# Performance work log

Hardware: AMD Instinct MI355X
Metric: run time of the kernel (lower is better)

Reference implementation:

```python
import jax, jax.numpy as jnp
import numpy as np

M1, M2, BS = 2000, 400, 8
AT = M1 + M2
E1, E2, E3 = 60000, 20000, 20000
H, F, NG, L, C = 64, 64, 50, 4, 4
CUTOFF = 10.0
LOG2 = 0.6931471805599453  # shift of ShiftedSoftplus


def _ssp(x):
    return jax.nn.softplus(x) - LOG2


def _smear(d):
    # GaussianSmearing(0, cutoff, NG)
    offset = jnp.linspace(0.0, CUTOFF, NG)
    coeff = -0.5 / (offset[1] - offset[0]) ** 2
    return jnp.exp(coeff * (d[:, None] - offset[None, :]) ** 2)  # [E, NG]


def _colored_mlp(attr, colors, w1, b1, w2, b2):
    # w1:[C,NG,F] b1:[C,F] w2:[C,F,F] b2:[C,F]; route each edge through its color's MLP
    out = jnp.zeros((attr.shape[0], w1.shape[-1]), attr.dtype)
    for c in range(C):  # fixed small color count
        h = _ssp(attr @ w1[c] + b1[c]) @ w2[c] + b2[c]
        out = out + jnp.where((colors == c)[:, None], h, jnp.zeros((), attr.dtype))
    return out


def _block(h, ei, ew, attr, col, p):
    # InteractionBlock: CFConv -> ssp -> linear
    mw1, mb1, mw2, mb2, cw1, cw2, cb2, bw, bb = p
    Ccut = 0.5 * (jnp.cos(ew * jnp.pi / CUTOFF) + 1.0)
    W = _colored_mlp(attr, col, mw1, mb1, mw2, mb2) * Ccut[:, None]  # [E,F]
    x = h @ cw1                                   # lin1 (no bias) [N,F]
    msg = x[ei[:, 0]] * W                         # gather x_j, modulate
    agg = jax.ops.segment_sum(msg, ei[:, 1], num_segments=h.shape[0])  # scatter-add
    x = agg @ cw2 + cb2                           # lin2
    return _ssp(x) @ bw + bb                      # act + block linear


def _batch_graph(ei, ew, col):
    # replicate per-structure edges across the batch with node offset b*AT
    offs = (jnp.arange(BS, dtype=ei.dtype) * AT)[:, None, None]
    ei_b = (ei[None] + offs).reshape(-1, 2)
    return ei_b, jnp.tile(ew, BS), jnp.tile(col, BS)


def _forward(sites, sites_p, e1, ew1, c1, e2, ew2, c2, e3, ew3, c3,
             emb_w, emb_p_w, mlp_w1, mlp_b1, mlp_w2, mlp_b2,
             conv_w1, conv_w2, conv_b2, blk_w, blk_b,
             out_w1, out_b1, out_w2, out_b2):
    h = jnp.concatenate([emb_w[sites], emb_p_w[sites_p]], axis=1).reshape(BS * AT, H)
    graphs = []
    for (ei, ew, col) in ((e1, ew1, c1), (e2, ew2, c2), (e3, ew3, c3)):
        ei_b, ew_b, col_b = _batch_graph(ei, ew, col)
        graphs.append((ei_b, ew_b, col_b, _smear(ew_b)))
    for l in range(L):
        delta = jnp.zeros_like(h)
        for g, (ei_b, ew_b, col_b, attr_b) in enumerate(graphs):
            p = (mlp_w1[l, g], mlp_b1[l, g], mlp_w2[l, g], mlp_b2[l, g],
                 conv_w1[l, g], conv_w2[l, g], conv_b2[l, g], blk_w[l, g], blk_b[l, g])
            delta = delta + _block(h, ei_b, ew_b, attr_b, col_b, p)
        h = h + delta
    hp = h.reshape(BS, AT, H)[:, M1:, :]   # mask selects pore nodes only
    o = hp @ out_w1 + out_b1               # NB: original has `h - self.act(h)` no-op, so no activation here
    o = o @ out_w2 + out_b2                # [BS, M2, 1]
    return o.sum(axis=1)                   # 'add' readout per batch -> [BS, 1]


def setup_inputs() -> dict:
    key = jax.random.key(0)
    ks = jax.random.split(key, 24)
    f = lambda i, shape, s=0.1: jax.random.normal(ks[i], shape, jnp.float32) * s
    sites = jax.random.randint(ks[0], (BS, M1), 0, 1, dtype=jnp.int32)
    sites_p = jax.random.randint(ks[1], (BS, M2), 0, 2, dtype=jnp.int32)
    e1 = jax.random.randint(ks[2], (E1, 2), 0, M1, dtype=jnp.int32)
    e2 = jnp.stack([jax.random.randint(ks[3], (E2,), 0, M1, dtype=jnp.int32),
                    jax.random.randint(ks[4], (E2,), M1, AT, dtype=jnp.int32)], 1)
    e3 = jnp.stack([jax.random.randint(ks[5], (E3,), M1, AT, dtype=jnp.int32),
                    jax.random.randint(ks[6], (E3,), 0, M1, dtype=jnp.int32)], 1)
    ew1 = jax.random.uniform(ks[7], (E1,), jnp.float32, 0.5, CUTOFF)
    ew2 = jax.random.uniform(ks[8], (E2,), jnp.float32, 0.5, CUTOFF)
    ew3 = jax.random.uniform(ks[9], (E3,), jnp.float32, 0.5, CUTOFF)
    c1 = jax.random.randint(ks[10], (E1,), 0, C, dtype=jnp.int32)
    c2 = jax.random.randint(ks[11], (E2,), 0, C, dtype=jnp.int32)
    c3 = jax.random.randint(ks[12], (E3,), 0, C, dtype=jnp.int32)
    return {
        'sites': sites, 'sites_p': sites_p,
        'edge_idx1': e1, 'edge_weight1': ew1, 'colors1': c1,
        'edge_idx2': e2, 'edge_weight2': ew2, 'colors2': c2,
        'edge_idx3': e3, 'edge_weight3': ew3, 'colors3': c3,
        'emb_w': f(13, (1, H), 1.0), 'emb_p_w': f(14, (2, H), 1.0),
        'mlp_w1': f(15, (L, 3, C, NG, F)), 'mlp_b1': jnp.zeros((L, 3, C, F), jnp.float32),
        'mlp_w2': f(16, (L, 3, C, F, F)), 'mlp_b2': jnp.zeros((L, 3, C, F), jnp.float32),
        'conv_w1': f(17, (L, 3, H, F)), 'conv_w2': f(18, (L, 3, F, H)),
        'conv_b2': jnp.zeros((L, 3, H), jnp.float32),
        'blk_w': f(19, (L, 3, H, H)), 'blk_b': jnp.zeros((L, 3, H), jnp.float32),
        'out_w1': f(20, (H, H // 2)), 'out_b1': jnp.zeros((H // 2,), jnp.float32),
        'out_w2': f(21, (H // 2, 1)), 'out_b2': jnp.zeros((1,), jnp.float32),
    }


def reference(sites, sites_p, edge_idx1, edge_weight1, colors1,
              edge_idx2, edge_weight2, colors2, edge_idx3, edge_weight3, colors3,
              emb_w, emb_p_w, mlp_w1, mlp_b1, mlp_w2, mlp_b2,
              conv_w1, conv_w2, conv_b2, blk_w, blk_b,
              out_w1, out_b1, out_w2, out_b2):
    return _forward(sites, sites_p, edge_idx1, edge_weight1, colors1,
                    edge_idx2, edge_weight2, colors2, edge_idx3, edge_weight3, colors3,
                    emb_w, emb_p_w, mlp_w1, mlp_b1, mlp_w2, mlp_b2,
                    conv_w1, conv_w2, conv_b2, blk_w, blk_b,
                    out_w1, out_b1, out_w2, out_b2)
```

## Files before the change

### kernel.cpp

```cpp
#include <hip/hip_runtime.h>
#include <math.h>

constexpr int M1 = 2000, M2 = 400, BS = 8;
constexpr int AT = M1 + M2;
constexpr int NN = BS * AT;
constexpr int E1 = 60000, E2 = 20000, E3 = 20000;
constexpr int ET = E1 + E2 + E3;
constexpr int H = 64, F = 64, NG = 50, L = 4, C = 4;
constexpr float CUTOFF = 10.0f;
constexpr float LOG2F_ = 0.6931471805599453f;

constexpr float SMEAR_STEP = 10.0f / 49.0f;
constexpr float SMEAR_COEFF = -12.005f;
constexpr float PI_OVER_CUT = 0.31415926535897932f;

constexpr int NBLK = (ET + 255) / 256;

constexpr int NT = 256;
constexpr float DSCALE = (float)(NT - 1) / CUTOFF;

constexpr int GP0 = E1 + 3 * M1;
constexpr int GP1 = E2 + 3 * M2;
constexpr int GP2 = E3 + 3 * M1;
constexpr int ETP = GP0 + GP1 + GP2;

constexpr int TILE_M = 32;

constexpr int GU  = 4400;
constexpr int GBLK = GU / 4;
constexpr int SITE_T = M1 / 4;
constexpr int PORE_T = M2 / 4;
constexpr int NTILE  = SITE_T + PORE_T;

constexpr int LT0 = M1 / 4;
constexpr int LT1 = M1 / 4;
constexpr int LT2 = M2 / 4;
constexpr int LTOT = LT0 + LT1 + LT2;
constexpr int PADB = (3 * AT + 255) / 256;

constexpr int A_TAB  = 192;
constexpr int A_INIT = NN * 64 / 256;
constexpr int A_CNT  = NBLK;
constexpr int A_CV   = 3;
constexpr int A_TOT  = A_TAB + A_INIT + A_CNT + A_CV;
constexpr int B_PACK = 48 * NT * 64 / 256;
constexpr int B_TOT  = B_PACK + 3;

constexpr size_t O_HA    = 0;
constexpr size_t O_HB    = O_HA  + (size_t)NN * 64 * 4;
constexpr size_t O_XG    = O_HB  + (size_t)NN * 64 * 4;
constexpr size_t O_MSG   = O_XG  + (size_t)3 * AT * 512 * 2;
constexpr size_t O_TABF  = O_MSG + (size_t)3 * 8 * AT * 64 * 4;
constexpr size_t O_TAB2  = O_TABF + (size_t)48 * NT * 64 * 4;
constexpr size_t O_EDATA = O_TAB2 + (size_t)48 * NT * 64 * 4;
constexpr size_t O_INT   = O_EDATA + (size_t)ETP * 16;
constexpr int I_DEG  = 0;
constexpr int I_CUR  = 7200;
constexpr int I_ZEND = 14400;
constexpr int I_BASE = 14400;
constexpr int I_CV   = 21616;

__device__ inline float sspf(float x) {
    return fmaxf(x, 0.0f) + log1pf(expf(-fabsf(x))) - LOG2F_;
}
__device__ inline float sspf_fast(float x) {
    float t = __expf(-fabsf(x));
    return fmaxf(x, 0.0f) + __logf(1.0f + t) - LOG2F_;
}

__device__ inline unsigned int bf16rn(float x) {
    unsigned int u = __float_as_uint(x);
    u = (u + 0x7FFFu + ((u >> 16) & 1u)) >> 16;
    return u & 0xFFFFu;
}

__device__ inline int graph_off(int g) { return g == 0 ? 0 : (g == 1 ? GP0 : GP0 + GP1); }

__device__ inline void edge_decode(int idx, int& g, int& e,
                                   const int* ei1, const int* ei2, const int* ei3,
                                   const int* c1, const int* c2, const int* c3,
                                   const int*& ei, const int*& cl) {
    if (idx < E1)            { g = 0; e = idx;           ei = ei1; cl = c1; }
    else if (idx < E1 + E2)  { g = 1; e = idx - E1;      ei = ei2; cl = c2; }
    else                     { g = 2; e = idx - E1 - E2; ei = ei3; cl = c3; }
}

__global__ __launch_bounds__(256) void k_setupA(
    const float* __restrict__ mlp_w1, const float* __restrict__ mlp_b1,
    const float* __restrict__ mlp_w2, const float* __restrict__ mlp_b2,
    float* __restrict__ tabF,
    const int* __restrict__ sites, const int* __restrict__ sites_p,
    const float* __restrict__ emb_w, const float* __restrict__ emb_p_w,
    float* __restrict__ h,
    const int* __restrict__ ei1, const int* __restrict__ ei2,
    const int* __restrict__ ei3, const int* __restrict__ c1,
    const int* __restrict__ c2, const int* __restrict__ c3,
    int* __restrict__ deg,
    const float* __restrict__ conv_b2, const float* __restrict__ blk_w,
    const float* __restrict__ blk_b, float* __restrict__ cvbuf) {
    int bid = blockIdx.x;
    int t = threadIdx.x;
    if (bid < A_TAB) {
        const int lane = t & 63;
        int wslot = bid * 4 + (t >> 6);
        int s = wslot >> 4;
        int pq = wslot & 15;
        int l = s % L;
        int gc = s / L;
        int c = gc % C;
        int g = gc / C;
        size_t wb = (size_t)((l * 3 + g) * C + c);
        const float* w1 = mlp_w1 + wb * NG * F;
        const float* w2 = mlp_w2 + wb * F * F;
        float w1c[NG], w2c[F];
        #pragma unroll
        for (int k = 0; k < NG; k++) w1c[k] = w1[k * F + lane];
        #pragma unroll
        for (int k = 0; k < F; k++) w2c[k] = w2[k * F + lane];
        float b1c = mlp_b1[wb * F + lane];
        float b2c = mlp_b2[wb * F + lane];
        for (int pp = 0; pp < 16; pp++) {
            int p = pq * 16 + pp;
            float d = (float)p * (CUTOFF / (float)(NT - 1));
            float dd = d - (float)lane * SMEAR_STEP;
            float av = (lane < NG) ? __expf(SMEAR_COEFF * dd * dd) : 0.0f;
            float acc = b1c;
            #pragma unroll
            for (int k = 0; k < NG; k++) acc = fmaf(__shfl(av, k), w1c[k], acc);
            float tt = sspf_fast(acc);
            float acc2 = b2c;
            #pragma unroll
            for (int j = 0; j < F; j++) acc2 = fmaf(__shfl(tt, j), w2c[j], acc2);
            float ccut = 0.5f * (__cosf(d * PI_OVER_CUT) + 1.0f);
            tabF[((size_t)s * NT + p) * 64 + lane] = acc2 * ccut;
        }
    } else if (bid < A_TAB + A_INIT) {
        int idx = (bid - A_TAB) * 256 + t;
        int f = idx & 63;
        int n = idx >> 6;
        int b = n / AT;
        int i = n - b * AT;
        float v;
        if (i < M1) v = emb_w[sites[b * M1 + i] * H + f];
        else        v = emb_p_w[sites_p[b * M2 + (i - M1)] * H + f];
        h[idx] = v;
    } else if (bid < A_TAB + A_INIT + A_CNT) {
        int idx = (bid - A_TAB - A_INIT) * 256 + t;
        if (idx < ET) {
            int g, e; const int* ei; const int* cl;
            edge_decode(idx, g, e, ei1, ei2, ei3, c1, c2, c3, ei, cl);
            atomicAdd(&deg[g * AT + ei[2 * e + 1]], 1);
        }
    } else {
        int s = (bid - A_TAB - A_INIT - A_CNT) * 4 + (t >> 6);
        int lane = t & 63;
        if (s < 12) {
            float sl = sspf(conv_b2[s * 64 + lane]);
            const float* bw = blk_w + (size_t)s * 4096;
            float a = blk_b[s * 64 + lane];
            #pragma unroll 8
            for (int k = 0; k < 64; k++)
                a = fmaf(__shfl(sl, k), bw[k * 64 + lane], a);
            cvbuf[s * 64 + lane] = a;
        }
    }
}

__global__ __launch_bounds__(256) void k_setupB(
    const float* __restrict__ tabF, unsigned int* __restrict__ tab2,
    const int* __restrict__ deg, int* __restrict__ base) {
    int bid = blockIdx.x;
    int t = threadIdx.x;
    if (bid < B_PACK) {
        int idx = bid * 256 + t;
        int pc = idx & (NT * 64 - 1);
        int nxt = (pc < (NT - 1) * 64) ? idx + 64 : idx;
        unsigned int lo = bf16rn(tabF[idx]);
        unsigned int hi = bf16rn(tabF[nxt]);
        tab2[idx] = lo | (hi << 16);
    } else {
        const int T = 256, CH = 10;
        __shared__ int lsum[256];
        int g = bid - B_PACK;
        int loc[CH];
        int s = 0;
        #pragma unroll
        for (int i = 0; i < CH; i++) {
            int idx = t * CH + i;
            int v = (idx < AT) ? ((deg[g * AT + idx] + 3) & ~3) : 0;
            loc[i] = s;
            s += v;
        }
        lsum[t] = s;
        __syncthreads();
        for (int off = 1; off < T; off <<= 1) {
            int v = 0;
            if (t >= off) v = lsum[t - off];
            __syncthreads();
            lsum[t] += v;
            __syncthreads();
        }
        int tb = lsum[t] - s;
        #pragma unroll
        for (int i = 0; i < CH; i++) {
            int idx = t * CH + i;
            if (idx < AT) base[g * (AT + 1) + idx] = tb + loc[i];
        }
        if (t == T - 1) base[g * (AT + 1) + AT] = lsum[T - 1];
    }
}

__device__ inline void fma4(float acc[4], float a, const float4 b) {
    acc[0] = fmaf(a, b.x, acc[0]);
    acc[1] = fmaf(a, b.y, acc[1]);
    acc[2] = fmaf(a, b.z, acc[2]);
    acc[3] = fmaf(a, b.w, acc[3]);
}

__device__ inline void stage_B(const float* __restrict__ gB, float (*Bs)[68], int t) {
    #pragma unroll
    for (int i = 0; i < 4; i++) {
        int v = t + i * 256;
        int r = v >> 4, c4 = (v & 15) * 4;
        *(float4*)&Bs[r][c4] = *(const float4*)(gB + (size_t)r * 64 + c4);
    }
}
struct WReg { float4 v0, v1, v2, v3; };
__device__ inline WReg stage_ld(const float* __restrict__ g, int t) {
    int r0 = t >> 4, c4 = (t & 15) * 4;
    WReg w;
    w.v0 = *(const float4*)(g + (size_t)r0 * 64 + c4);
    w.v1 = *(const float4*)(g + (size_t)(r0 + 16) * 64 + c4);
    w.v2 = *(const float4*)(g + (size_t)(r0 + 32) * 64 + c4);
    w.v3 = *(const float4*)(g + (size_t)(r0 + 48) * 64 + c4);
    return w;
}
__device__ inline void stage_st(const WReg& w, float (*Bs)[68], int t) {
    int r0 = t >> 4, c4 = (t & 15) * 4;
    *(float4*)&Bs[r0][c4]      = w.v0;
    *(float4*)&Bs[r0 + 16][c4] = w.v1;
    *(float4*)&Bs[r0 + 32][c4] = w.v2;
    *(float4*)&Bs[r0 + 48][c4] = w.v3;
}

__device__ inline void gemm_tile(const float (*As)[68], const float (*Bs)[68],
                                 int r0, int c0, float acc0[4], float acc1[4]) {
    #pragma unroll 4
    for (int k0 = 0; k0 < 64; k0 += 4) {
        float4 a0 = *(const float4*)&As[r0][k0];
        float4 a1 = *(const float4*)&As[r0 + 1][k0];
        float4 b0 = *(const float4*)&Bs[k0][c0];
        float4 b1 = *(const float4*)&Bs[k0 + 1][c0];
        float4 b2 = *(const float4*)&Bs[k0 + 2][c0];
        float4 b3 = *(const float4*)&Bs[k0 + 3][c0];
        fma4(acc0, a0.x, b0); fma4(acc0, a0.y, b1);
        fma4(acc0, a0.z, b2); fma4(acc0, a0.w, b3);
        fma4(acc1, a1.x, b0); fma4(acc1, a1.y, b1);
        fma4(acc1, a1.z, b2); fma4(acc1, a1.w, b3);
    }
}

__device__ inline void xg_transpose_store(const float (*T)[68],
                                          unsigned short* __restrict__ xg,
                                          int g, int i0, int t) {
    int k = t >> 6, c = t & 63;
    unsigned int w0 = bf16rn(T[k * 8 + 0][c]) | (bf16rn(T[k * 8 + 1][c]) << 16);
    unsigned int w1 = bf16rn(T[k * 8 + 2][c]) | (bf16rn(T[k * 8 + 3][c]) << 16);
    unsigned int w2 = bf16rn(T[k * 8 + 4][c]) | (bf16rn(T[k * 8 + 5][c]) << 16);
    unsigned int w3 = bf16rn(T[k * 8 + 6][c]) | (bf16rn(T[k * 8 + 7][c]) << 16);
    unsigned short* out = xg + (((size_t)g * AT + i0 + k) * 64 + c) * 8;
    *(uint4*)out = make_uint4(w0, w1, w2, w3);
}

__device__ inline float tab_lerp(unsigned int u, int z) {
    float lo = __uint_as_float(u << 16);
    float hi = __uint_as_float(u & 0xFFFF0000u);
    return fmaf(__int_as_float(z), hi - lo, lo);
}
__device__ inline void gmadd8(float acc[8], uint4 q, float wl) {
    acc[0] = fmaf(__uint_as_float(q.x << 16),         wl, acc[0]);
    acc[1] = fmaf(__uint_as_float(q.x & 0xFFFF0000u), wl, acc[1]);
    acc[2] = fmaf(__uint_as_float(q.y << 16),         wl, acc[2]);
    acc[3] = fmaf(__uint_as_float(q.y & 0xFFFF0000u), wl, acc[3]);
    acc[4] = fmaf(__uint_as_float(q.z << 16),         wl, acc[4]);
    acc[5] = fmaf(__uint_as_float(q.z & 0xFFFF0000u), wl, acc[5]);
    acc[6] = fmaf(__uint_as_float(q.w << 16),         wl, acc[6]);
    acc[7] = fmaf(__uint_as_float(q.w & 0xFFFF0000u), wl, acc[7]);
}

__global__ __launch_bounds__(256) void k_gather(
    const int4* __restrict__ edata, const int* __restrict__ base,
    const unsigned int* __restrict__ tab2,
    const unsigned short* __restrict__ xg,
    float* __restrict__ msg, int l) {
    const int t = threadIdx.x;
    const int lane = t & 63;
    const int u = blockIdx.x * 4 + (t >> 6);
    int g, dst;
    if (u < M1)           { g = 0; dst = u; }
    else if (u < AT)      { g = 1; dst = u; }
    else                  { g = 2; dst = u - AT; }
    const int s = base[g * (AT + 1) + dst];
    const int e = base[g * (AT + 1) + dst + 1];
    const int4* ed = edata + graph_off(g);
    const unsigned int* tg = tab2 + ((size_t)g * C * L + l) * NT * 64;
    const unsigned short* xgg = xg + (size_t)g * AT * 512;
    float acc[8];
    #pragma unroll
    for (int j = 0; j < 8; j++) acc[j] = 0.0f;
    for (int i = s; i < e; i += 4) {
        int4 e0 = ed[i];
        int4 e1 = ed[i + 1];
        int4 e2 = ed[i + 2];
        int4 e3 = ed[i + 3];
        unsigned int u0 = tg[(size_t)e0.y * 64 + lane];
        unsigned int u1 = tg[(size_t)e1.y * 64 + lane];
        unsigned int u2 = tg[(size_t)e2.y * 64 + lane];
        unsigned int u3 = tg[(size_t)e3.y * 64 + lane];
        uint4 q0 = *(const uint4*)(xgg + ((size_t)e0.x * 64 + lane) * 8);
        uint4 q1 = *(const uint4*)(xgg + ((size_t)e1.x * 64 + lane) * 8);
        uint4 q2 = *(const uint4*)(xgg + ((size_t)e2.x * 64 + lane) * 8);
        uint4 q3 = *(const uint4*)(xgg + ((size_t)e3.x * 64 + lane) * 8);
        gmadd8(acc, q0, tab_lerp(u0, e0.z));
        gmadd8(acc, q1, tab_lerp(u1, e1.z));
        gmadd8(acc, q2, tab_lerp(u2, e2.z));
        gmadd8(acc, q3, tab_lerp(u3, e3.z));
    }
    float* mp = msg + ((size_t)g * 8 * AT + dst) * 64 + lane;
    #pragma unroll
    for (int b = 0; b < 8; b++) mp[(size_t)b * AT * 64] = acc[b];
}

__global__ __launch_bounds__(256) void k_node(
    const float* __restrict__ msg,
    const float* __restrict__ conv_w2, const float* __restrict__ conv_b2,
    const float* __restrict__ blk_w, const float* __restrict__ blk_b,
    const float* __restrict__ conv_w1, const float* __restrict__ cvbuf,
    const float* __restrict__ hIn, float* __restrict__ hOut,
    unsigned short* __restrict__ xg, int l, int last) {
    __shared__ float As[TILE_M][68];
    __shared__ float Ps[TILE_M][68];
    __shared__ float Bs[64][68];
    const int t = threadIdx.x;
    const int bid = blockIdx.x;
    const int site = (bid < SITE_T) ? 1 : 0;
    const int i0 = site ? bid * 4 : M1 + (bid - SITE_T) * 4;
    const int gA = site ? 0 : 1;
    const size_t pbA = (size_t)(l * 3 + gA);
    const size_t pbB = (size_t)(l * 3 + 2);

    WReg R = stage_ld(conv_w2 + pbA * 4096, t);
    #pragma unroll
    for (int it = 0; it < 2; it++) {
        int v = t + it * 256;
        int r = v >> 4, c4 = (v & 15) * 4;
        int k = r >> 3, b = r & 7;
        *(float4*)&As[r][c4] =
            *(const float4*)(msg + (((size_t)gA * 8 + b) * AT + i0 + k) * 64 + c4);
    }
    stage_st(R, Bs, t);
    R = stage_ld(blk_w + pbA * 4096, t);
    __syncthreads();

    const int cg = t & 15, rg = t >> 4;
    const int c0 = cg * 4, r0 = rg * 2;
    const float* cvl = cvbuf + (size_t)l * 3 * 64;

    float4 cb = *(const float4*)(conv_b2 + pbA * 64 + c0);
    float x0[4] = {cb.x, cb.y, cb.z, cb.w};
    float x1[4] = {cb.x, cb.y, cb.z, cb.w};
    gemm_tile(As, Bs, r0, c0, x0, x1);
    __syncthreads();
    *(float4*)&As[r0][c0] =
        make_float4(sspf(x0[0]), sspf(x0[1]), sspf(x0[2]), sspf(x0[3]));
    *(float4*)&As[r0 + 1][c0] =
        make_float4(sspf(x1[0]), sspf(x1[1]), sspf(x1[2]), sspf(x1[3]));
    stage_st(R, Bs, t);
    if (site) R = stage_ld(conv_w2 + pbB * 4096, t);
    else if (!last) R = stage_ld(conv_w1 + (size_t)((l + 1) * 3 + 2) * 4096, t);
    __syncthreads();

    const int k0r = r0 >> 3, b0r = r0 & 7;
    const size_t o0 = ((size_t)b0r * AT + i0 + k0r) * 64 + c0;
    const int k1r = (r0 + 1) >> 3, b1r = (r0 + 1) & 7;
    const size_t o1 = ((size_t)b1r * AT + i0 + k1r) * 64 + c0;
    float4 h0 = *(const float4*)(hIn + o0);
    float4 h1 = *(const float4*)(hIn + o1);
    float4 bbA = *(const float4*)(blk_b + pbA * 64 + c0);
    float4 ex;
    if (site) {
        float4 bbB = *(const float4*)(blk_b + pbB * 64 + c0);
        float4 cv1 = *(const float4*)(cvl + 64 + c0);
        ex = make_float4(bbB.x + cv1.x, bbB.y + cv1.y, bbB.z + cv1.z, bbB.w + cv1.w);
    } else {
        float4 cv0 = *(const float4*)(cvl + c0);
        float4 cv2 = *(const float4*)(cvl + 128 + c0);
        ex = make_float4(cv0.x + cv2.x, cv0.y + cv2.y, cv0.z + cv2.z, cv0.w + cv2.w);
    }
    float d0[4] = {h0.x + bbA.x + ex.x, h0.y + bbA.y + ex.y,
                   h0.z + bbA.z + ex.z, h0.w + bbA.w + ex.w};
    float d1[4] = {h1.x + bbA.x + ex.x, h1.y + bbA.y + ex.y,
                   h1.z + bbA.z + ex.z, h1.w + bbA.w + ex.w};
    gemm_tile(As, Bs, r0, c0, d0, d1);

    if (site) {
        __syncthreads();
        #pragma unroll
        for (int it = 0; it < 2; it++) {
            int v = t + it * 256;
            int r = v >> 4, c4 = (v & 15) * 4;
            int k = r >> 3, b = r & 7;
            *(float4*)&As[r][c4] =
                *(const float4*)(msg + (((size_t)2 * 8 + b) * AT + i0 + k) * 64 + c4);
        }
        stage_st(R, Bs, t);
        R = stage_ld(blk_w + pbB * 4096, t);
        __syncthreads();
        float4 cb2v = *(const float4*)(conv_b2 + pbB * 64 + c0);
        float y0[4] = {cb2v.x, cb2v.y, cb2v.z, cb2v.w};
        float y1[4] = {cb2v.x, cb2v.y, cb2v.z, cb2v.w};
        gemm_tile(As, Bs, r0, c0, y0, y1);
        __syncthreads();
        *(float4*)&As[r0][c0] =
            make_float4(sspf(y0[0]), sspf(y0[1]), sspf(y0[2]), sspf(y0[3]));
        *(float4*)&As[r0 + 1][c0] =
            make_float4(sspf(y1[0]), sspf(y1[1]), sspf(y1[2]), sspf(y1[3]));
        stage_st(R, Bs, t);
        if (!last) R = stage_ld(conv_w1 + (size_t)((l + 1) * 3 + 0) * 4096, t);
        __syncthreads();
        gemm_tile(As, Bs, r0, c0, d0, d1);
    }
    *(float4*)(hOut + o0) = make_float4(d0[0], d0[1], d0[2], d0[3]);
    *(float4*)(hOut + o1) = make_float4(d1[0], d1[1], d1[2], d1[3]);
    if (last) return;

    __syncthreads();
    *(float4*)&As[r0][c0]     = make_float4(d0[0], d0[1], d0[2], d0[3]);
    *(float4*)&As[r0 + 1][c0] = make_float4(d1[0], d1[1], d1[2], d1[3]);
    stage_st(R, Bs, t);
    if (site) R = stage_ld(conv_w1 + (size_t)((l + 1) * 3 + 1) * 4096, t);
    __syncthreads();
    float p0[4] = {0, 0, 0, 0}, p1[4] = {0, 0, 0, 0};
    gemm_tile(As, Bs, r0, c0, p0, p1);
    __syncthreads();
    *(float4*)&Ps[r0][c0]     = make_float4(p0[0], p0[1], p0[2], p0[3]);
    *(float4*)&Ps[r0 + 1][c0] = make_float4(p1[0], p1[1], p1[2], p1[3]);
    if (site) stage_st(R, Bs, t);
    __syncthreads();
    xg_transpose_store(Ps, xg, site ? 0 : 2, i0, t);
    if (site) {
        float q0[4] = {0, 0, 0, 0}, q1[4] = {0, 0, 0, 0};
        gemm_tile(As, Bs, r0, c0, q0, q1);
        __syncthreads();
        *(float4*)&Ps[r0][c0]     = make_float4(q0[0], q0[1], q0[2], q0[3]);
        *(float4*)&Ps[r0 + 1][c0] = make_float4(q1[0], q1[1], q1[2], q1[3]);
        __syncthreads();
        xg_transpose_store(Ps, xg, 1, i0, t);
    }
}

__global__ __launch_bounds__(256) void k_fl(
    const int* __restrict__ ei1, const int* __restrict__ ei2,
    const int* __restrict__ ei3, const int* __restrict__ c1,
    const int* __restrict__ c2, const int* __restrict__ c3,
    const float* __restrict__ ew1, const float* __restrict__ ew2,
    const float* __restrict__ ew3,
    const int* __restrict__ base, int* __restrict__ cur,
    const int* __restrict__ deg, int4* __restrict__ edata,
    const float* __restrict__ h, const float* __restrict__ conv_w1,
    unsigned short* __restrict__ xg) {
    __shared__ float As[TILE_M][68];
    __shared__ float Bs[64][68];
    int t = threadIdx.x;
    if (blockIdx.x >= LTOT + NBLK) {
        int idx = (blockIdx.x - LTOT - NBLK) * 256 + t;
        if (idx >= 3 * AT) return;
        int g = idx / AT, dn = idx - g * AT;
        int d = deg[g * AT + dn];
        int pd = (d + 3) & ~3;
        int4* ep = edata + graph_off(g) + base[g * (AT + 1) + dn] + d;
        for (int k2 = 0; k2 < pd - d; k2++) ep[k2] = make_int4(0, NT - 1, 0, 0);
        return;
    }
    if (blockIdx.x >= LTOT) {
        int idx = (blockIdx.x - LTOT) * 256 + t;
        if (idx >= ET) return;
        int g, e; const int* ei; const int* cl;
        edge_decode(idx, g, e, ei1, ei2, ei3, c1, c2, c3, ei, cl);
        const float* ew = (g == 0) ? ew1 : (g == 1 ? ew2 : ew3);
        int dst = ei[2 * e + 1];
        int src = ei[2 * e];
        int p = base[g * (AT + 1) + dst] + atomicAdd(&cur[g * AT + dst], 1);
        float tt = ew[e] * DSCALE;
        int i0 = min((int)tt, NT - 2);
        float fr = tt - (float)i0;
        int cb = cl[e] * (L * NT) + i0;
        edata[graph_off(g) + p] = make_int4(src, cb, __float_as_int(fr), 0);
        return;
    }
    int g, igrp;
    {
        int bid = blockIdx.x;
        if (bid < LT0)            { g = 0; igrp = bid; }
        else if (bid < LT0 + LT1) { g = 1; igrp = bid - LT0; }
        else                      { g = 2; igrp = LT0 + (bid - LT0 - LT1); }
    }
    int i0 = igrp * 4;
    #pragma unroll
    for (int it = 0; it < 2; it++) {
        int v = t + it * 256;
        int r = v >> 4, c4 = (v & 15) * 4;
        int n = (r & 7) * AT + i0 + (r >> 3);
        *(float4*)&As[r][c4] = *(const float4*)(h + (size_t)n * 64 + c4);
    }
    stage_B(conv_w1 + (size_t)g * 4096, Bs, t);
    __syncthreads();
    int cg = t & 15, rg = t >> 4;
    int c0 = cg * 4, r0 = rg * 2;
    float acc0[4] = {0, 0, 0, 0}, acc1[4] = {0, 0, 0, 0};
    gemm_tile(As, Bs, r0, c0, acc0, acc1);
    __syncthreads();
    *(float4*)&As[r0][c0]     = make_float4(acc0[0], acc0[1], acc0[2], acc0[3]);
    *(float4*)&As[r0 + 1][c0] = make_float4(acc1[0], acc1[1], acc1[2], acc1[3]);
    __syncthreads();
    xg_transpose_store(As, xg, g, i0, t);
}

__global__ void k_read(const float* __restrict__ h,
                       const float* __restrict__ w1, const float* __restrict__ b1,
                       const float* __restrict__ w2, const float* __restrict__ b2,
                       float* __restrict__ out) {
    int b = blockIdx.x;
    int lane = threadIdx.x & 63;
    int wv = threadIdx.x >> 6;
    __shared__ float part[4];
    float weff = 0.0f;
    #pragma unroll
    for (int j = 0; j < H / 2; j++) weff = fmaf(w1[lane * (H / 2) + j], w2[j], weff);
    float acc = 0.0f;
    for (int i = wv * (M2 / 4); i < (wv + 1) * (M2 / 4); i++)
        acc += h[((size_t)b * AT + M1 + i) * H + lane];
    float v = acc * weff;
    for (int off = 32; off; off >>= 1) v += __shfl_xor(v, off);
    if (lane == 0) part[wv] = v;
    __syncthreads();
    if (threadIdx.x == 0) {
        float bias = b2[0];
        for (int j = 0; j < H / 2; j++) bias = fmaf(b1[j], w2[j], bias);
        out[b] = part[0] + part[1] + part[2] + part[3] + (float)M2 * bias;
    }
}

extern "C" void kernel_launch(void* const* d_in, const int* in_sizes, int n_in,
                              void* d_out, int out_size, void* d_ws, size_t ws_size,
                              hipStream_t stream) {
    const int* sites   = (const int*)d_in[0];
    const int* sites_p = (const int*)d_in[1];
    const int* ei1 = (const int*)d_in[2];
    const float* ew1 = (const float*)d_in[3];
    const int* c1 = (const int*)d_in[4];
    const int* ei2 = (const int*)d_in[5];
    const float* ew2 = (const float*)d_in[6];
    const int* c2 = (const int*)d_in[7];
    const int* ei3 = (const int*)d_in[8];
    const float* ew3 = (const float*)d_in[9];
    const int* c3 = (const int*)d_in[10];
    const float* emb_w   = (const float*)d_in[11];
    const float* emb_p_w = (const float*)d_in[12];
    const float* mlp_w1 = (const float*)d_in[13];
    const float* mlp_b1 = (const float*)d_in[14];
    const float* mlp_w2 = (const float*)d_in[15];
    const float* mlp_b2 = (const float*)d_in[16];
    const float* conv_w1 = (const float*)d_in[17];
    const float* conv_w2 = (const float*)d_in[18];
    const float* conv_b2 = (const float*)d_in[19];
    const float* blk_w = (const float*)d_in[20];
    const float* blk_b = (const float*)d_in[21];
    const float* out_w1 = (const float*)d_in[22];
    const float* out_b1 = (const float*)d_in[23];
    const float* out_w2 = (const float*)d_in[24];
    const float* out_b2 = (const float*)d_in[25];

    char* ws = (char*)d_ws;
    float* hA   = (float*)(ws + O_HA);
    float* hB   = (float*)(ws + O_HB);
    unsigned short* xg = (unsigned short*)(ws + O_XG);
    float* msg  = (float*)(ws + O_MSG);
    float* tabF = (float*)(ws + O_TABF);
    unsigned int* tab2 = (unsigned int*)(ws + O_TAB2);
    int4*  edata = (int4*)(ws + O_EDATA);
    int* ip    = (int*)(ws + O_INT);
    int* deg   = ip + I_DEG;
    int* cur   = ip + I_CUR;
    int* ibase = ip + I_BASE;
    float* cvbuf = (float*)(ip + I_CV);

    hipMemsetAsync(ip, 0, (size_t)I_ZEND * sizeof(int), stream);

    k_setupA<<<A_TOT, 256, 0, stream>>>(mlp_w1, mlp_b1, mlp_w2, mlp_b2, tabF,
                                        sites, sites_p, emb_w, emb_p_w, hA,
                                        ei1, ei2, ei3, c1, c2, c3, deg,
                                        conv_b2, blk_w, blk_b, cvbuf);
    k_setupB<<<B_TOT, 256, 0, stream>>>(tabF, tab2, deg, ibase);
    k_fl<<<LTOT + NBLK + PADB, 256, 0, stream>>>(ei1, ei2, ei3, c1, c2, c3,
                                                 ew1, ew2, ew3, ibase, cur, deg,
                                                 edata, hA, conv_w1, xg);

    float* hcur = hA;
    float* hnxt = hB;
    for (int l = 0; l < L; l++) {
        int last = (l == L - 1) ? 1 : 0;
        k_gather<<<GBLK, 256, 0, stream>>>(edata, ibase, tab2, xg, msg, l);
        k_node<<<NTILE, 256, 0, stream>>>(msg, conv_w2, conv_b2, blk_w, blk_b,
                                          conv_w1, cvbuf, hcur, hnxt, xg, l, last);
        float* tmp = hcur; hcur = hnxt; hnxt = tmp;
    }
    k_read<<<BS, 256, 0, stream>>>(hcur, out_w1, out_b1, out_w2, out_b2, (float*)d_out);
}
```

Measured before the change: 327.1 us.

## Split gather per batch half, fuse table bf16 packing into table kernel

The gather kernel now assigns two wavefronts per destination node, each handling four of the eight batch copies with 8-byte loads, and unrolls the edge loop by eight with a four-edge tail. Edge bounds are made wave-uniform with readfirstlane. The filter-table kernel computes 17 points per wave and writes the packed bf16 pair table directly, removing the fp32 intermediate table and its separate packing pass. The degree scan becomes its own small kernel. The price is that each edge's table entry and edge record are loaded twice, once per half, while the gather gets twice as many waves to hide latency.

```diff
diff --git a/kernel.cpp b/kernel.cpp
--- a/kernel.cpp
+++ b/kernel.cpp
@@ -26,8 +26,7 @@
 
 constexpr int TILE_M = 32;
 
-constexpr int GU  = 4400;
-constexpr int GBLK = GU / 4;
+constexpr int GUB = 8800 / 4;
 constexpr int SITE_T = M1 / 4;
 constexpr int PORE_T = M2 / 4;
 constexpr int NTILE  = SITE_T + PORE_T;
@@ -42,16 +41,13 @@
 constexpr int A_INIT = NN * 64 / 256;
 constexpr int A_CNT  = NBLK;
 constexpr int A_CV   = 3;
-constexpr int A_TOT  = A_TAB + A_INIT + A_CNT + A_CV;
-constexpr int B_PACK = 48 * NT * 64 / 256;
-constexpr int B_TOT  = B_PACK + 3;
+constexpr int A_TOT  = A_INIT + A_CNT + A_CV;
 
 constexpr size_t O_HA    = 0;
 constexpr size_t O_HB    = O_HA  + (size_t)NN * 64 * 4;
 constexpr size_t O_XG    = O_HB  + (size_t)NN * 64 * 4;
 constexpr size_t O_MSG   = O_XG  + (size_t)3 * AT * 512 * 2;
-constexpr size_t O_TABF  = O_MSG + (size_t)3 * 8 * AT * 64 * 4;
-constexpr size_t O_TAB2  = O_TABF + (size_t)48 * NT * 64 * 4;
+constexpr size_t O_TAB2  = O_MSG + (size_t)3 * 8 * AT * 64 * 4;
 constexpr size_t O_EDATA = O_TAB2 + (size_t)48 * NT * 64 * 4;
 constexpr size_t O_INT   = O_EDATA + (size_t)ETP * 16;
 constexpr int I_DEG  = 0;
@@ -85,10 +81,54 @@
     else                     { g = 2; e = idx - E1 - E2; ei = ei3; cl = c3; }
 }
 
-__global__ __launch_bounds__(256) void k_setupA(
+__global__ __launch_bounds__(256) void k_tab(
     const float* __restrict__ mlp_w1, const float* __restrict__ mlp_b1,
     const float* __restrict__ mlp_w2, const float* __restrict__ mlp_b2,
-    float* __restrict__ tabF,
+    unsigned int* __restrict__ tab2) {
+    const int t = threadIdx.x;
+    const int lane = t & 63;
+    int wslot = blockIdx.x * 4 + (t >> 6);
+    int s = wslot >> 4;
+    int pq = wslot & 15;
+    int l = s % L;
+    int gc = s / L;
+    int c = gc % C;
+    int g = gc / C;
+    size_t wb = (size_t)((l * 3 + g) * C + c);
+    const float* w1 = mlp_w1 + wb * NG * F;
+    const float* w2 = mlp_w2 + wb * F * F;
+    float w1c[NG], w2c[F];
+    #pragma unroll
+    for (int k = 0; k < NG; k++) w1c[k] = w1[k * F + lane];
+    #pragma unroll
+    for (int k = 0; k < F; k++) w2c[k] = w2[k * F + lane];
+    float b1c = mlp_b1[wb * F + lane];
+    float b2c = mlp_b2[wb * F + lane];
+    float vals[17];
+    for (int pp = 0; pp <= 16; pp++) {
+        int p = min(pq * 16 + pp, NT - 1);
+        float d = (float)p * (CUTOFF / (float)(NT - 1));
+        float dd = d - (float)lane * SMEAR_STEP;
+        float av = (lane < NG) ? __expf(SMEAR_COEFF * dd * dd) : 0.0f;
+        float acc = b1c;
+        #pragma unroll
+        for (int k = 0; k < NG; k++) acc = fmaf(__shfl(av, k), w1c[k], acc);
+        float tt = sspf_fast(acc);
+        float acc2 = b2c;
+        #pragma unroll
+        for (int j = 0; j < F; j++) acc2 = fmaf(__shfl(tt, j), w2c[j], acc2);
+        float ccut = 0.5f * (__cosf(d * PI_OVER_CUT) + 1.0f);
+        vals[pp] = acc2 * ccut;
+    }
+    #pragma unroll
+    for (int pp = 0; pp < 16; pp++) {
+        int p = pq * 16 + pp;
+        tab2[((size_t)s * NT + p) * 64 + lane] =
+            bf16rn(vals[pp]) | (bf16rn(vals[pp + 1]) << 16);
+    }
+}
+
+__global__ __launch_bounds__(256) void k_setupA(
     const int* __restrict__ sites, const int* __restrict__ sites_p,
     const float* __restrict__ emb_w, const float* __restrict__ emb_p_w,
     float* __restrict__ h,
@@ -100,42 +140,8 @@
     const float* __restrict__ blk_b, float* __restrict__ cvbuf) {
     int bid = blockIdx.x;
     int t = threadIdx.x;
-    if (bid < A_TAB) {
-        const int lane = t & 63;
-        int wslot = bid * 4 + (t >> 6);
-        int s = wslot >> 4;
-        int pq = wslot & 15;
-        int l = s % L;
-        int gc = s / L;
-        int c = gc % C;
-        int g = gc / C;
-        size_t wb = (size_t)((l * 3 + g) * C + c);
-        const float* w1 = mlp_w1 + wb * NG * F;
-        const float* w2 = mlp_w2 + wb * F * F;
-        float w1c[NG], w2c[F];
-        #pragma unroll
-        for (int k = 0; k < NG; k++) w1c[k] = w1[k * F + lane];
-        #pragma unroll
-        for (int k = 0; k < F; k++) w2c[k] = w2[k * F + lane];
-        float b1c = mlp_b1[wb * F + lane];
-        float b2c = mlp_b2[wb * F + lane];
-        for (int pp = 0; pp < 16; pp++) {
-            int p = pq * 16 + pp;
-            float d = (float)p * (CUTOFF / (float)(NT - 1));
-            float dd = d - (float)lane * SMEAR_STEP;
-            float av = (lane < NG) ? __expf(SMEAR_COEFF * dd * dd) : 0.0f;
-            float acc = b1c;
-            #pragma unroll
-            for (int k = 0; k < NG; k++) acc = fmaf(__shfl(av, k), w1c[k], acc);
-            float tt = sspf_fast(acc);
-            float acc2 = b2c;
-            #pragma unroll
-            for (int j = 0; j < F; j++) acc2 = fmaf(__shfl(tt, j), w2c[j], acc2);
-            float ccut = 0.5f * (__cosf(d * PI_OVER_CUT) + 1.0f);
-            tabF[((size_t)s * NT + p) * 64 + lane] = acc2 * ccut;
-        }
-    } else if (bid < A_TAB + A_INIT) {
-        int idx = (bid - A_TAB) * 256 + t;
+    if (bid < A_INIT) {
+        int idx = bid * 256 + t;
         int f = idx & 63;
         int n = idx >> 6;
         int b = n / AT;
@@ -144,15 +150,15 @@
         if (i < M1) v = emb_w[sites[b * M1 + i] * H + f];
         else        v = emb_p_w[sites_p[b * M2 + (i - M1)] * H + f];
         h[idx] = v;
-    } else if (bid < A_TAB + A_INIT + A_CNT) {
-        int idx = (bid - A_TAB - A_INIT) * 256 + t;
+    } else if (bid < A_INIT + A_CNT) {
+        int idx = (bid - A_INIT) * 256 + t;
         if (idx < ET) {
             int g, e; const int* ei; const int* cl;
             edge_decode(idx, g, e, ei1, ei2, ei3, c1, c2, c3, ei, cl);
             atomicAdd(&deg[g * AT + ei[2 * e + 1]], 1);
         }
     } else {
-        int s = (bid - A_TAB - A_INIT - A_CNT) * 4 + (t >> 6);
+        int s = (bid - A_INIT - A_CNT) * 4 + (t >> 6);
         int lane = t & 63;
         if (s < 12) {
             float sl = sspf(conv_b2[s * 64 + lane]);
@@ -166,48 +172,37 @@
     }
 }
 
-__global__ __launch_bounds__(256) void k_setupB(
-    const float* __restrict__ tabF, unsigned int* __restrict__ tab2,
+__global__ __launch_bounds__(256) void k_scan(
     const int* __restrict__ deg, int* __restrict__ base) {
-    int bid = blockIdx.x;
+    const int T = 256, CH = 10;
+    __shared__ int lsum[256];
+    int g = blockIdx.x;
     int t = threadIdx.x;
-    if (bid < B_PACK) {
-        int idx = bid * 256 + t;
-        int pc = idx & (NT * 64 - 1);
-        int nxt = (pc < (NT - 1) * 64) ? idx + 64 : idx;
-        unsigned int lo = bf16rn(tabF[idx]);
-        unsigned int hi = bf16rn(tabF[nxt]);
-        tab2[idx] = lo | (hi << 16);
-    } else {
-        const int T = 256, CH = 10;
-        __shared__ int lsum[256];
-        int g = bid - B_PACK;
-        int loc[CH];
-        int s = 0;
-        #pragma unroll
-        for (int i = 0; i < CH; i++) {
-            int idx = t * CH + i;
-            int v = (idx < AT) ? ((deg[g * AT + idx] + 3) & ~3) : 0;
-            loc[i] = s;
-            s += v;
-        }
-        lsum[t] = s;
-        __syncthreads();
-        for (int off = 1; off < T; off <<= 1) {
-            int v = 0;
-            if (t >= off) v = lsum[t - off];
-            __syncthreads();
-            lsum[t] += v;
-            __syncthreads();
-        }
-        int tb = lsum[t] - s;
-        #pragma unroll
-        for (int i = 0; i < CH; i++) {
-            int idx = t * CH + i;
-            if (idx < AT) base[g * (AT + 1) + idx] = tb + loc[i];
-        }
-        if (t == T - 1) base[g * (AT + 1) + AT] = lsum[T - 1];
-    }
+    int loc[CH];
+    int s = 0;
+    #pragma unroll
+    for (int i = 0; i < CH; i++) {
+        int idx = t * CH + i;
+        int v = (idx < AT) ? ((deg[g * AT + idx] + 3) & ~3) : 0;
+        loc[i] = s;
+        s += v;
+    }
+    lsum[t] = s;
+    __syncthreads();
+    for (int off = 1; off < T; off <<= 1) {
+        int v = 0;
+        if (t >= off) v = lsum[t - off];
+        __syncthreads();
+        lsum[t] += v;
+        __syncthreads();
+    }
+    int tb = lsum[t] - s;
+    #pragma unroll
+    for (int i = 0; i < CH; i++) {
+        int idx = t * CH + i;
+        if (idx < AT) base[g * (AT + 1) + idx] = tb + loc[i];
+    }
+    if (t == T - 1) base[g * (AT + 1) + AT] = lsum[T - 1];
 }
 
 __device__ inline void fma4(float acc[4], float a, const float4 b) {
@@ -216,7 +211,6 @@
     acc[2] = fmaf(a, b.z, acc[2]);
     acc[3] = fmaf(a, b.w, acc[3]);
 }
-
 __device__ inline void stage_B(const float* __restrict__ gB, float (*Bs)[68], int t) {
     #pragma unroll
     for (int i = 0; i < 4; i++) {
@@ -242,7 +236,6 @@
     *(float4*)&Bs[r0 + 32][c4] = w.v2;
     *(float4*)&Bs[r0 + 48][c4] = w.v3;
 }
-
 __device__ inline void gemm_tile(const float (*As)[68], const float (*Bs)[68],
                                  int r0, int c0, float acc0[4], float acc1[4]) {
     #pragma unroll 4
@@ -259,7 +252,6 @@
         fma4(acc1, a1.z, b2); fma4(acc1, a1.w, b3);
     }
 }
-
 __device__ inline void xg_transpose_store(const float (*T)[68],
                                           unsigned short* __restrict__ xg,
                                           int g, int i0, int t) {
@@ -271,21 +263,16 @@
     unsigned short* out = xg + (((size_t)g * AT + i0 + k) * 64 + c) * 8;
     *(uint4*)out = make_uint4(w0, w1, w2, w3);
 }
-
 __device__ inline float tab_lerp(unsigned int u, int z) {
     float lo = __uint_as_float(u << 16);
     float hi = __uint_as_float(u & 0xFFFF0000u);
     return fmaf(__int_as_float(z), hi - lo, lo);
 }
-__device__ inline void gmadd8(float acc[8], uint4 q, float wl) {
+__device__ inline void gmadd4(float acc[4], uint2 q, float wl) {
     acc[0] = fmaf(__uint_as_float(q.x << 16),         wl, acc[0]);
     acc[1] = fmaf(__uint_as_float(q.x & 0xFFFF0000u), wl, acc[1]);
     acc[2] = fmaf(__uint_as_float(q.y << 16),         wl, acc[2]);
     acc[3] = fmaf(__uint_as_float(q.y & 0xFFFF0000u), wl, acc[3]);
-    acc[4] = fmaf(__uint_as_float(q.z << 16),         wl, acc[4]);
-    acc[5] = fmaf(__uint_as_float(q.z & 0xFFFF0000u), wl, acc[5]);
-    acc[6] = fmaf(__uint_as_float(q.w << 16),         wl, acc[6]);
-    acc[7] = fmaf(__uint_as_float(q.w & 0xFFFF0000u), wl, acc[7]);
 }
 
 __global__ __launch_bounds__(256) void k_gather(
@@ -296,39 +283,68 @@
     const int t = threadIdx.x;
     const int lane = t & 63;
     const int u = blockIdx.x * 4 + (t >> 6);
+    const int gd = u >> 1;
+    const int bh = u & 1;
     int g, dst;
-    if (u < M1)           { g = 0; dst = u; }
-    else if (u < AT)      { g = 1; dst = u; }
-    else                  { g = 2; dst = u - AT; }
-    const int s = base[g * (AT + 1) + dst];
-    const int e = base[g * (AT + 1) + dst + 1];
+    if (gd < M1)      { g = 0; dst = gd; }
+    else if (gd < AT) { g = 1; dst = gd; }
+    else              { g = 2; dst = gd - AT; }
+    const int s = __builtin_amdgcn_readfirstlane(base[g * (AT + 1) + dst]);
+    const int e = __builtin_amdgcn_readfirstlane(base[g * (AT + 1) + dst + 1]);
     const int4* ed = edata + graph_off(g);
     const unsigned int* tg = tab2 + ((size_t)g * C * L + l) * NT * 64;
-    const unsigned short* xgg = xg + (size_t)g * AT * 512;
-    float acc[8];
-    #pragma unroll
-    for (int j = 0; j < 8; j++) acc[j] = 0.0f;
-    for (int i = s; i < e; i += 4) {
-        int4 e0 = ed[i];
-        int4 e1 = ed[i + 1];
-        int4 e2 = ed[i + 2];
-        int4 e3 = ed[i + 3];
-        unsigned int u0 = tg[(size_t)e0.y * 64 + lane];
-        unsigned int u1 = tg[(size_t)e1.y * 64 + lane];
-        unsigned int u2 = tg[(size_t)e2.y * 64 + lane];
-        unsigned int u3 = tg[(size_t)e3.y * 64 + lane];
-        uint4 q0 = *(const uint4*)(xgg + ((size_t)e0.x * 64 + lane) * 8);
-        uint4 q1 = *(const uint4*)(xgg + ((size_t)e1.x * 64 + lane) * 8);
-        uint4 q2 = *(const uint4*)(xgg + ((size_t)e2.x * 64 + lane) * 8);
-        uint4 q3 = *(const uint4*)(xgg + ((size_t)e3.x * 64 + lane) * 8);
-        gmadd8(acc, q0, tab_lerp(u0, e0.z));
-        gmadd8(acc, q1, tab_lerp(u1, e1.z));
-        gmadd8(acc, q2, tab_lerp(u2, e2.z));
-        gmadd8(acc, q3, tab_lerp(u3, e3.z));
-    }
-    float* mp = msg + ((size_t)g * 8 * AT + dst) * 64 + lane;
-    #pragma unroll
-    for (int b = 0; b < 8; b++) mp[(size_t)b * AT * 64] = acc[b];
+    const unsigned short* xgg = xg + (size_t)g * AT * 512 + bh * 4;
+    float acc[4] = {0.0f, 0.0f, 0.0f, 0.0f};
+    int i = s;
+    for (; i + 8 <= e; i += 8) {
+        int4 E0 = ed[i];     int4 E1 = ed[i + 1];
+        int4 E2 = ed[i + 2]; int4 E3 = ed[i + 3];
+        int4 E4 = ed[i + 4]; int4 E5 = ed[i + 5];
+        int4 E6 = ed[i + 6]; int4 E7 = ed[i + 7];
+        unsigned int u0 = tg[(size_t)E0.y * 64 + lane];
+        unsigned int u1 = tg[(size_t)E1.y * 64 + lane];
+        unsigned int u2 = tg[(size_t)E2.y * 64 + lane];
+        unsigned int u3 = tg[(size_t)E3.y * 64 + lane];
+        unsigned int u4 = tg[(size_t)E4.y * 64 + lane];
+        unsigned int u5 = tg[(size_t)E5.y * 64 + lane];
+        unsigned int u6 = tg[(size_t)E6.y * 64 + lane];
+        unsigned int u7 = tg[(size_t)E7.y * 64 + lane];
+        uint2 q0 = *(const uint2*)(xgg + ((size_t)E0.x * 64 + lane) * 8);
+        uint2 q1 = *(const uint2*)(xgg + ((size_t)E1.x * 64 + lane) * 8);
+        uint2 q2 = *(const uint2*)(xgg + ((size_t)E2.x * 64 + lane) * 8);
+        uint2 q3 = *(const uint2*)(xgg + ((size_t)E3.x * 64 + lane) * 8);
+        uint2 q4 = *(const uint2*)(xgg + ((size_t)E4.x * 64 + lane) * 8);
+        uint2 q5 = *(const uint2*)(xgg + ((size_t)E5.x * 64 + lane) * 8);
+        uint2 q6 = *(const uint2*)(xgg + ((size_t)E6.x * 64 + lane) * 8);
+        uint2 q7 = *(const uint2*)(xgg + ((size_t)E7.x * 64 + lane) * 8);
+        gmadd4(acc, q0, tab_lerp(u0, E0.z));
+        gmadd4(acc, q1, tab_lerp(u1, E1.z));
+        gmadd4(acc, q2, tab_lerp(u2, E2.z));
+        gmadd4(acc, q3, tab_lerp(u3, E3.z));
+        gmadd4(acc, q4, tab_lerp(u4, E4.z));
+        gmadd4(acc, q5, tab_lerp(u5, E5.z));
+        gmadd4(acc, q6, tab_lerp(u6, E6.z));
+        gmadd4(acc, q7, tab_lerp(u7, E7.z));
+    }
+    if (i < e) {
+        int4 E0 = ed[i];     int4 E1 = ed[i + 1];
+        int4 E2 = ed[i + 2]; int4 E3 = ed[i + 3];
+        unsigned int u0 = tg[(size_t)E0.y * 64 + lane];
+        unsigned int u1 = tg[(size_t)E1.y * 64 + lane];
+        unsigned int u2 = tg[(size_t)E2.y * 64 + lane];
+        unsigned int u3 = tg[(size_t)E3.y * 64 + lane];
+        uint2 q0 = *(const uint2*)(xgg + ((size_t)E0.x * 64 + lane) * 8);
+        uint2 q1 = *(const uint2*)(xgg + ((size_t)E1.x * 64 + lane) * 8);
+        uint2 q2 = *(const uint2*)(xgg + ((size_t)E2.x * 64 + lane) * 8);
+        uint2 q3 = *(const uint2*)(xgg + ((size_t)E3.x * 64 + lane) * 8);
+        gmadd4(acc, q0, tab_lerp(u0, E0.z));
+        gmadd4(acc, q1, tab_lerp(u1, E1.z));
+        gmadd4(acc, q2, tab_lerp(u2, E2.z));
+        gmadd4(acc, q3, tab_lerp(u3, E3.z));
+    }
+    float* mp = msg + (((size_t)g * 8 + bh * 4) * AT + dst) * 64 + lane;
+    #pragma unroll
+    for (int b = 0; b < 4; b++) mp[(size_t)b * AT * 64] = acc[b];
 }
 
 __global__ __launch_bounds__(256) void k_node(
@@ -586,7 +602,6 @@
     float* hB   = (float*)(ws + O_HB);
     unsigned short* xg = (unsigned short*)(ws + O_XG);
     float* msg  = (float*)(ws + O_MSG);
-    float* tabF = (float*)(ws + O_TABF);
     unsigned int* tab2 = (unsigned int*)(ws + O_TAB2);
     int4*  edata = (int4*)(ws + O_EDATA);
     int* ip    = (int*)(ws + O_INT);
@@ -597,11 +612,11 @@
 
     hipMemsetAsync(ip, 0, (size_t)I_ZEND * sizeof(int), stream);
 
-    k_setupA<<<A_TOT, 256, 0, stream>>>(mlp_w1, mlp_b1, mlp_w2, mlp_b2, tabF,
-                                        sites, sites_p, emb_w, emb_p_w, hA,
+    k_tab<<<A_TAB, 256, 0, stream>>>(mlp_w1, mlp_b1, mlp_w2, mlp_b2, tab2);
+    k_setupA<<<A_TOT, 256, 0, stream>>>(sites, sites_p, emb_w, emb_p_w, hA,
                                         ei1, ei2, ei3, c1, c2, c3, deg,
                                         conv_b2, blk_w, blk_b, cvbuf);
-    k_setupB<<<B_TOT, 256, 0, stream>>>(tabF, tab2, deg, ibase);
+    k_scan<<<3, 256, 0, stream>>>(deg, ibase);
     k_fl<<<LTOT + NBLK + PADB, 256, 0, stream>>>(ei1, ei2, ei3, c1, c2, c3,
                                                  ew1, ew2, ew3, ibase, cur, deg,
                                                  edata, hA, conv_w1, xg);
@@ -610,7 +625,7 @@
     float* hnxt = hB;
     for (int l = 0; l < L; l++) {
         int last = (l == L - 1) ? 1 : 0;
-        k_gather<<<GBLK, 256, 0, stream>>>(edata, ibase, tab2, xg, msg, l);
+        k_gather<<<GUB, 256, 0, stream>>>(edata, ibase, tab2, xg, msg, l);
         k_node<<<NTILE, 256, 0, stream>>>(msg, conv_w2, conv_b2, blk_w, blk_b,
                                           conv_w1, cvbuf, hcur, hnxt, xg, l, last);
         float* tmp = hcur; hcur = hnxt; hnxt = tmp;
```

After: 341.9 us. 1.05x slower.
